# Kernel tuning notes

Measured on AMD Instinct MI355X. Metric: run time of the kernel, lower is better.

The kernel has to match this reference:

```python
import jax, jax.numpy as jnp
import numpy as np

N_USERS = 100000
N_ITEMS = 50000
EMB_DIM = 64
N_LAYERS = 2
N_INTENTS = 128
N_EDGES = 4000000
N_NODES = N_USERS + N_ITEMS


def setup_inputs() -> dict:
    key = jax.random.key(0)
    k1, k2, k3, k4, k5 = jax.random.split(key, 5)
    return {
        "user_emb": 0.1 * jax.random.normal(k1, (N_USERS, EMB_DIM), dtype=jnp.float32),
        "item_emb": 0.1 * jax.random.normal(k2, (N_ITEMS, EMB_DIM), dtype=jnp.float32),
        "intents": jax.random.normal(k3, (EMB_DIM, N_INTENTS), dtype=jnp.float32) * (2.0 / (EMB_DIM + N_INTENTS)) ** 0.5,
        "h_idx": jax.random.randint(k4, (N_EDGES,), 0, N_NODES, dtype=jnp.int64)
        if jax.config.jax_enable_x64 else jax.random.randint(k4, (N_EDGES,), 0, N_NODES, dtype=jnp.int32),
        "t_idx": jax.random.randint(k5, (N_EDGES,), 0, N_NODES, dtype=jnp.int32),
    }


def _spmm(h_idx, t_idx, g_vals, x):
    # y[h] += g_vals * x[t]  (sparse matrix @ dense, COO form)
    gathered = x[t_idx] * g_vals[:, None]  # [E, D]
    return jax.ops.segment_sum(gathered, h_idx, num_segments=N_NODES)


def reference(user_emb, item_emb, intents, h_idx, t_idx):
    # --- _cal_sparse_adj: G = D^{-1/2} A D^{-1/2}, A values are ones ---
    deg = jax.ops.segment_sum(jnp.ones_like(h_idx, dtype=user_emb.dtype), h_idx,
                              num_segments=N_NODES)
    d_inv_sqrt = jnp.where(deg > 0, jax.lax.rsqrt(jnp.maximum(deg, 1e-12)), 0.0)
    g_vals = d_inv_sqrt[h_idx] * d_inv_sqrt[t_idx]  # [E]

    # --- multi-layer propagation with intent-aware embeddings ---
    embs = jnp.concatenate([user_emb, item_emb], axis=0)  # [N, D]
    all_embs = [embs]
    for _ in range(N_LAYERS):
        gnn_embs = _spmm(h_idx, t_idx, g_vals, embs)  # [N, D]
        # intent projection: softmax over intents, reconstruct in emb space
        u, it = embs[:N_USERS], embs[N_USERS:]
        u_int = jax.nn.softmax(u @ intents, axis=1) @ intents.T      # [n_users, D]
        i_int = jax.nn.softmax(it @ intents, axis=1) @ intents.T     # [n_items, D]
        int_embs = jnp.concatenate([u_int, i_int], axis=0)
        embs = gnn_embs + int_embs
        all_embs.append(embs)
    out = jnp.sum(jnp.stack(all_embs, axis=1), axis=1) / len(all_embs)  # mean over layers
    return out
```

## Files before the change

### kernel.cpp

```cpp
#include <hip/hip_runtime.h>
#include <math.h>

#define N_USERS 100000
#define N_ITEMS 50000
#define N_NODES 150000
#define EMB 64
#define NI 128
#define NUM_EDGES 4000000
#define NPAD 150016
#define NB 1172
#define BSTRIDE 4352
#define ETILE 8192
#define EGRID ((NUM_EDGES + ETILE - 1) / ETILE)
#define NT_ALL (NPAD / 16)
#define SBLK (NT_ALL / 4)
#define SENT 150000u

typedef __attribute__((ext_vector_type(8))) short bf16x8;
typedef __attribute__((ext_vector_type(4))) float f32x4;

__device__ __forceinline__ unsigned short f2bf(float f) {
    unsigned int u = __float_as_uint(f);
    u += 0x7FFFu + ((u >> 16) & 1u);
    return (unsigned short)(u >> 16);
}
__device__ __forceinline__ float bflo(unsigned int u) { return __uint_as_float(u << 16); }
__device__ __forceinline__ float bfhi(unsigned int u) { return __uint_as_float(u & 0xFFFF0000u); }


__global__ __launch_bounds__(512) void bucket_scatter(const int* __restrict__ h,
                                                      const int* __restrict__ t,
                                                      int* __restrict__ gcur,
                                                      unsigned int* __restrict__ ebuf) {
    __shared__ int lc[NB];
    __shared__ int lbase[NB];
    __shared__ int lcur[NB];
    int tid = threadIdx.x;
    for (int i = tid; i < NB; i += 512) lc[i] = 0;
    __syncthreads();
    int base = blockIdx.x * ETILE;
#pragma unroll
    for (int k = 0; k < ETILE / 512; ++k) {
        int idx = base + k * 512 + tid;
        if (idx < NUM_EDGES) atomicAdd(&lc[h[idx] >> 7], 1);
    }
    __syncthreads();
    for (int i = tid; i < NB; i += 512) {
        int c = lc[i];
        lbase[i] = c ? (i * BSTRIDE + atomicAdd(&gcur[i], c)) : 0;
        lcur[i] = 0;
    }
    __syncthreads();
#pragma unroll
    for (int k = 0; k < ETILE / 512; ++k) {
        int idx = base + k * 512 + tid;
        if (idx < NUM_EDGES) {
            int hh = h[idx], tt = t[idx];
            int b = hh >> 7;
            int p = lbase[b] + atomicAdd(&lcur[b], 1);
            int lim = b * BSTRIDE + BSTRIDE - 1;
            p = (p <= lim) ? p : lim;
            ebuf[p] = ((unsigned int)(hh & 127) << 18) | (unsigned int)tt;
        }
    }
}


__global__ __launch_bounds__(512) void bucket_csr(const int* __restrict__ gcur,
                                                  unsigned int* __restrict__ ebuf,
                                                  int2* __restrict__ rmeta,
                                                  float* __restrict__ dinv,
                                                  int* __restrict__ perm) {
    __shared__ unsigned int in_s[BSTRIDE];
    __shared__ int cnt_s[128];
    __shared__ int base_s[128];
    __shared__ int sc[128];
    __shared__ int dg[128];
    int b = blockIdx.x, tid = threadIdx.x;
    int s = b * BSTRIDE;
    int n = gcur[b];
    if (n > BSTRIDE) n = BSTRIDE;

    for (int i = tid; i < n; i += 512) in_s[i] = ebuf[s + i];
    if (tid < 128) cnt_s[tid] = 0;
    __syncthreads();
    for (int i = tid; i < n; i += 512) atomicAdd(&cnt_s[in_s[i] >> 18], 1);
    __syncthreads();

    int c = 0, pc = 0;
    if (tid < 128) {
        c = cnt_s[tid];
        pc = (c + 3) & ~3;
        sc[tid] = pc;
        dg[tid] = c;
    }
    __syncthreads();
    for (int off = 1; off < 128; off <<= 1) {
        int tv = 0;
        if (tid < 128 && tid >= off) tv = sc[tid - off];
        __syncthreads();
        if (tid < 128 && tid >= off) sc[tid] += tv;
        __syncthreads();
    }
    if (tid < 128) {
        int excl = sc[tid] - pc;
        base_s[tid] = excl;
        int node = (b << 7) + tid;
        rmeta[node] = make_int2(s + excl, pc);
        dinv[node] = (c > 0) ? rsqrtf((float)c) : 0.0f;
        int tb = tid & ~15;
        int rank = 0;
#pragma unroll
        for (int j = 0; j < 16; ++j) {
            int dj = dg[tb + j];
            rank += (dj > c) || (dj == c && (tb + j) < tid);
        }
        perm[(b << 7) + tb + rank] = node;
        for (int p2 = c; p2 < pc; ++p2) ebuf[s + excl + p2] = SENT;
        cnt_s[tid] = 0;
    }
    __syncthreads();
    for (int i = tid; i < n; i += 512) {
        unsigned int qv = in_s[i];
        int hl = (int)(qv >> 18);
        int p = base_s[hl] + atomicAdd(&cnt_s[hl], 1);
        ebuf[s + p] = qv & 0x3FFFFu;
    }
}


__global__ void init_kernel(const float4* __restrict__ ue4, const float4* __restrict__ ie4,
                            uint2* __restrict__ ebf4, float4* __restrict__ out4) {
    int i = blockIdx.x * blockDim.x + threadIdx.x;
    const int uelems = N_USERS * EMB / 4;
    const int relems = N_NODES * EMB / 4;
    const int total  = NPAD * EMB / 4;
    if (i < total) {
        float4 v = make_float4(0.f, 0.f, 0.f, 0.f);
        if (i < uelems) v = ue4[i];
        else if (i < relems) v = ie4[i - uelems];
        if (i < relems) out4[i] = v;
        unsigned int p0 = ((unsigned int)f2bf(v.y) << 16) | f2bf(v.x);
        unsigned int p1 = ((unsigned int)f2bf(v.w) << 16) | f2bf(v.z);
        ebf4[i] = make_uint2(p0, p1);
    }
}


__global__ __launch_bounds__(256) void wconv(const float* __restrict__ W,
                                             unsigned short* __restrict__ Wt,
                                             unsigned short* __restrict__ W2b) {
    int i = blockIdx.x * 256 + threadIdx.x;
    if (i < EMB * NI) {
        int d = i >> 7, c = i & 127;
        unsigned short b = f2bf(W[i]);
        W2b[i] = b;
        Wt[c * EMB + d] = b;
    }
}


__global__ __launch_bounds__(256, 7) void spmm_intent(const int2* __restrict__ rmeta,
                                                      const unsigned int* __restrict__ col,
                                                      const float* __restrict__ dinv,
                                                      const int* __restrict__ perm,
                                                      const unsigned short* __restrict__ ebf,
                                                      unsigned short* __restrict__ ebfout,
                                                      const unsigned short* __restrict__ Wt,
                                                      const unsigned short* __restrict__ W2b,
                                                      float* __restrict__ acc, float scale) {
    __shared__ __align__(16) float UPool[4][1408];

    int tid = threadIdx.x;
    int wid = tid >> 6, lane = tid & 63;
    int q = lane >> 4, c = lane & 15;
    int qq = lane >> 3, cc = lane & 7;
    int tile = blockIdx.x * 4 + wid;
    if (tile >= NT_ALL) return;
    int rowbase = tile << 4;
    float* fw = &UPool[wid][0];
    unsigned short* pw = (unsigned short*)&UPool[wid][1088];

#pragma unroll 1
    for (int half = 0; half < 2; ++half) {
        int prow = perm[rowbase + half * 8 + qq];
        int2 rm = rmeta[prow];
        int s = rm.x, pcv = rm.y;
        float dr = dinv[prow];

        float a0 = 0.f, a1 = 0.f, a2 = 0.f, a3 = 0.f;
        float a4 = 0.f, a5 = 0.f, a6 = 0.f, a7 = 0.f;
        const unsigned short* eb = ebf + (cc << 3);

        int e0 = (int)(col[s]     & 0x3FFFFu);
        int e1 = (int)(col[s + 1] & 0x3FFFFu);
        int e2 = (int)(col[s + 2] & 0x3FFFFu);
        int e3 = (int)(col[s + 3] & 0x3FFFFu);
        float g0 = dinv[e0], g1 = dinv[e1], g2 = dinv[e2], g3 = dinv[e3];
        uint4 u0 = *(const uint4*)(eb + ((size_t)e0 << 6));
        uint4 u1 = *(const uint4*)(eb + ((size_t)e1 << 6));
        uint4 u2 = *(const uint4*)(eb + ((size_t)e2 << 6));
        uint4 u3 = *(const uint4*)(eb + ((size_t)e3 << 6));
        int f0 = (int)(col[s + 4] & 0x3FFFFu);
        int f1 = (int)(col[s + 5] & 0x3FFFFu);
        int f2 = (int)(col[s + 6] & 0x3FFFFu);
        int f3 = (int)(col[s + 7] & 0x3FFFFu);

        for (int it = 0; it < pcv; it += 4) {
            float h0 = dinv[f0], h1 = dinv[f1], h2 = dinv[f2], h3 = dinv[f3];
            uint4 v0 = *(const uint4*)(eb + ((size_t)f0 << 6));
            uint4 v1 = *(const uint4*)(eb + ((size_t)f1 << 6));
            uint4 v2 = *(const uint4*)(eb + ((size_t)f2 << 6));
            uint4 v3 = *(const uint4*)(eb + ((size_t)f3 << 6));
            int x0 = (int)(col[s + it + 8]  & 0x3FFFFu);
            int x1 = (int)(col[s + it + 9]  & 0x3FFFFu);
            int x2 = (int)(col[s + it + 10] & 0x3FFFFu);
            int x3 = (int)(col[s + it + 11] & 0x3FFFFu);
            a0 = fmaf(g0, bflo(u0.x), a0); a1 = fmaf(g0, bfhi(u0.x), a1);
            a2 = fmaf(g0, bflo(u0.y), a2); a3 = fmaf(g0, bfhi(u0.y), a3);
            a4 = fmaf(g0, bflo(u0.z), a4); a5 = fmaf(g0, bfhi(u0.z), a5);
            a6 = fmaf(g0, bflo(u0.w), a6); a7 = fmaf(g0, bfhi(u0.w), a7);
            a0 = fmaf(g1, bflo(u1.x), a0); a1 = fmaf(g1, bfhi(u1.x), a1);
            a2 = fmaf(g1, bflo(u1.y), a2); a3 = fmaf(g1, bfhi(u1.y), a3);
            a4 = fmaf(g1, bflo(u1.z), a4); a5 = fmaf(g1, bfhi(u1.z), a5);
            a6 = fmaf(g1, bflo(u1.w), a6); a7 = fmaf(g1, bfhi(u1.w), a7);
            a0 = fmaf(g2, bflo(u2.x), a0); a1 = fmaf(g2, bfhi(u2.x), a1);
            a2 = fmaf(g2, bflo(u2.y), a2); a3 = fmaf(g2, bfhi(u2.y), a3);
            a4 = fmaf(g2, bflo(u2.z), a4); a5 = fmaf(g2, bfhi(u2.z), a5);
            a6 = fmaf(g2, bflo(u2.w), a6); a7 = fmaf(g2, bfhi(u2.w), a7);
            a0 = fmaf(g3, bflo(u3.x), a0); a1 = fmaf(g3, bfhi(u3.x), a1);
            a2 = fmaf(g3, bflo(u3.y), a2); a3 = fmaf(g3, bfhi(u3.y), a3);
            a4 = fmaf(g3, bflo(u3.z), a4); a5 = fmaf(g3, bfhi(u3.z), a5);
            a6 = fmaf(g3, bflo(u3.w), a6); a7 = fmaf(g3, bfhi(u3.w), a7);
            u0 = v0; u1 = v1; u2 = v2; u3 = v3;
            g0 = h0; g1 = h1; g2 = h2; g3 = h3;
            f0 = x0; f1 = x1; f2 = x2; f3 = x3;
        }
        int fb = (half * 8 + qq) * 68 + (cc << 3);
        fw[fb + 0] = a0 * dr; fw[fb + 1] = a1 * dr;
        fw[fb + 2] = a2 * dr; fw[fb + 3] = a3 * dr;
        fw[fb + 4] = a4 * dr; fw[fb + 5] = a5 * dr;
        fw[fb + 6] = a6 * dr; fw[fb + 7] = a7 * dr;
    }

    int arow = perm[rowbase + c];
    const unsigned short* erow = ebf + ((size_t)arow << 6);
    bf16x8 A0 = *(const bf16x8*)(erow + (q << 3));
    bf16x8 A1 = *(const bf16x8*)(erow + 32 + (q << 3));
    f32x4 S[8];
#pragma unroll
    for (int t = 0; t < 8; ++t) {
        bf16x8 B0 = *(const bf16x8*)&Wt[(16 * t + c) * EMB + (q << 3)];
        bf16x8 B1 = *(const bf16x8*)&Wt[(16 * t + c) * EMB + 32 + (q << 3)];
        f32x4 z = {0.f, 0.f, 0.f, 0.f};
        z = __builtin_amdgcn_mfma_f32_16x16x32_bf16(A0, B0, z, 0, 0, 0);
        S[t] = __builtin_amdgcn_mfma_f32_16x16x32_bf16(A1, B1, z, 0, 0, 0);
    }

#pragma unroll
    for (int r = 0; r < 4; ++r) {
        float m = S[0][r];
#pragma unroll
        for (int t = 1; t < 8; ++t) m = fmaxf(m, S[t][r]);
        m = fmaxf(m, __shfl_xor(m, 1)); m = fmaxf(m, __shfl_xor(m, 2));
        m = fmaxf(m, __shfl_xor(m, 4)); m = fmaxf(m, __shfl_xor(m, 8));
        float sum = 0.f;
#pragma unroll
        for (int t = 0; t < 8; ++t) { float ex = __expf(S[t][r] - m); S[t][r] = ex; sum += ex; }
        sum += __shfl_xor(sum, 1); sum += __shfl_xor(sum, 2);
        sum += __shfl_xor(sum, 4); sum += __shfl_xor(sum, 8);
        float inv = 1.0f / sum;
#pragma unroll
        for (int t = 0; t < 8; ++t) S[t][r] *= inv;
    }

    f32x4 O0 = {0.f, 0.f, 0.f, 0.f}, O1 = O0, O2 = O0, O3 = O0;
#pragma unroll
    for (int s2 = 0; s2 < 4; ++s2) {
#pragma unroll
        for (int h2 = 0; h2 < 2; ++h2) {
            int t = 2 * s2 + h2;
#pragma unroll
            for (int r = 0; r < 4; ++r) {
                float p = S[t][r];
                unsigned short b = f2bf(p);
                pw[(4 * q + r) * 40 + (h2 << 4) + c] = b;
                S[t][r] = p - bflo((unsigned int)b);
            }
        }
        bf16x8 Pf = *(const bf16x8*)&pw[c * 40 + (q << 3)];
        {
            bf16x8 Bf0 = *(const bf16x8*)&W2b[(c) * NI + (s2 << 5) + (q << 3)];
            bf16x8 Bf1 = *(const bf16x8*)&W2b[(16 + c) * NI + (s2 << 5) + (q << 3)];
            O0 = __builtin_amdgcn_mfma_f32_16x16x32_bf16(Pf, Bf0, O0, 0, 0, 0);
            O1 = __builtin_amdgcn_mfma_f32_16x16x32_bf16(Pf, Bf1, O1, 0, 0, 0);
            bf16x8 Bf2 = *(const bf16x8*)&W2b[(32 + c) * NI + (s2 << 5) + (q << 3)];
            bf16x8 Bf3 = *(const bf16x8*)&W2b[(48 + c) * NI + (s2 << 5) + (q << 3)];
            O2 = __builtin_amdgcn_mfma_f32_16x16x32_bf16(Pf, Bf2, O2, 0, 0, 0);
            O3 = __builtin_amdgcn_mfma_f32_16x16x32_bf16(Pf, Bf3, O3, 0, 0, 0);
        }
#pragma unroll
        for (int h2 = 0; h2 < 2; ++h2) {
            int t = 2 * s2 + h2;
#pragma unroll
            for (int r = 0; r < 4; ++r)
                pw[(4 * q + r) * 40 + (h2 << 4) + c] = f2bf(S[t][r]);
        }
        bf16x8 Pl = *(const bf16x8*)&pw[c * 40 + (q << 3)];
        {
            bf16x8 Bf0 = *(const bf16x8*)&W2b[(c) * NI + (s2 << 5) + (q << 3)];
            bf16x8 Bf1 = *(const bf16x8*)&W2b[(16 + c) * NI + (s2 << 5) + (q << 3)];
            O0 = __builtin_amdgcn_mfma_f32_16x16x32_bf16(Pl, Bf0, O0, 0, 0, 0);
            O1 = __builtin_amdgcn_mfma_f32_16x16x32_bf16(Pl, Bf1, O1, 0, 0, 0);
            bf16x8 Bf2 = *(const bf16x8*)&W2b[(32 + c) * NI + (s2 << 5) + (q << 3)];
            bf16x8 Bf3 = *(const bf16x8*)&W2b[(48 + c) * NI + (s2 << 5) + (q << 3)];
            O2 = __builtin_amdgcn_mfma_f32_16x16x32_bf16(Pl, Bf2, O2, 0, 0, 0);
            O3 = __builtin_amdgcn_mfma_f32_16x16x32_bf16(Pl, Bf3, O3, 0, 0, 0);
        }
    }

    asm volatile("" ::: "memory");

#pragma unroll
    for (int r = 0; r < 4; ++r) {
        int rl = 4 * q + r;
        float* gr = &fw[rl * 68];
        gr[c]      += O0[r];
        gr[16 + c] += O1[r];
        gr[32 + c] += O2[r];
        gr[48 + c] += O3[r];
    }

    {
        int j = lane >> 2, sg = lane & 3;
        int rw = perm[rowbase + j];
        const float* gr = &fw[j * 68 + (sg << 4)];
        float4 x0 = *(const float4*)&gr[0];
        float4 x1 = *(const float4*)&gr[4];
        float4 x2 = *(const float4*)&gr[8];
        float4 x3 = *(const float4*)&gr[12];
        size_t base = ((size_t)rw << 6) + (sg << 4);
        uint4 w0, w1;
        w0.x = (unsigned int)f2bf(x0.x) | ((unsigned int)f2bf(x0.y) << 16);
        w0.y = (unsigned int)f2bf(x0.z) | ((unsigned int)f2bf(x0.w) << 16);
        w0.z = (unsigned int)f2bf(x1.x) | ((unsigned int)f2bf(x1.y) << 16);
        w0.w = (unsigned int)f2bf(x1.z) | ((unsigned int)f2bf(x1.w) << 16);
        w1.x = (unsigned int)f2bf(x2.x) | ((unsigned int)f2bf(x2.y) << 16);
        w1.y = (unsigned int)f2bf(x2.z) | ((unsigned int)f2bf(x2.w) << 16);
        w1.z = (unsigned int)f2bf(x3.x) | ((unsigned int)f2bf(x3.y) << 16);
        w1.w = (unsigned int)f2bf(x3.z) | ((unsigned int)f2bf(x3.w) << 16);
        *(uint4*)(ebfout + base) = w0;
        *(uint4*)(ebfout + base + 8) = w1;
        if (rw < N_NODES) {
            float4* ap = (float4*)(acc + base);
            float4 b0 = ap[0], b1 = ap[1], b2 = ap[2], b3 = ap[3];
            b0.x = (b0.x + x0.x) * scale; b0.y = (b0.y + x0.y) * scale;
            b0.z = (b0.z + x0.z) * scale; b0.w = (b0.w + x0.w) * scale;
            b1.x = (b1.x + x1.x) * scale; b1.y = (b1.y + x1.y) * scale;
            b1.z = (b1.z + x1.z) * scale; b1.w = (b1.w + x1.w) * scale;
            b2.x = (b2.x + x2.x) * scale; b2.y = (b2.y + x2.y) * scale;
            b2.z = (b2.z + x2.z) * scale; b2.w = (b2.w + x2.w) * scale;
            b3.x = (b3.x + x3.x) * scale; b3.y = (b3.y + x3.y) * scale;
            b3.z = (b3.z + x3.z) * scale; b3.w = (b3.w + x3.w) * scale;
            ap[0] = b0; ap[1] = b1; ap[2] = b2; ap[3] = b3;
        }
    }
}


extern "C" void kernel_launch(void* const* d_in, const int* in_sizes, int n_in,
                              void* d_out, int out_size, void* d_ws, size_t ws_size,
                              hipStream_t stream) {
    const float* ue = (const float*)d_in[0];
    const float* ie = (const float*)d_in[1];
    const float* W  = (const float*)d_in[2];
    const int*   h  = (const int*)d_in[3];
    const int*   t  = (const int*)d_in[4];
    float* out = (float*)d_out;

    int*            gcur  = (int*)d_ws;
    int2*           rmeta = (int2*)(gcur + 2048);
    float*          dinv  = (float*)(rmeta + NPAD);
    int*            perm  = (int*)(dinv + NPAD);
    unsigned short* ebfA  = (unsigned short*)(perm + NPAD);
    unsigned short* ebfB  = ebfA + (size_t)NPAD * EMB;
    unsigned int*   ebuf  = (unsigned int*)(ebfB + (size_t)NPAD * EMB);
    unsigned short* Wt    = (unsigned short*)(ebuf + NB * BSTRIDE + 16);
    unsigned short* W2b   = Wt + EMB * NI;

    hipMemsetAsync(gcur, 0, NB * sizeof(int), stream);
    hipMemsetAsync(ebuf + NB * BSTRIDE, 0, 16 * sizeof(unsigned int), stream);
    bucket_scatter<<<EGRID, 512, 0, stream>>>(h, t, gcur, ebuf);
    bucket_csr<<<NB, 512, 0, stream>>>(gcur, ebuf, rmeta, dinv, perm);
    init_kernel<<<(NPAD * EMB / 4 + 255) / 256, 256, 0, stream>>>(
        (const float4*)ue, (const float4*)ie, (uint2*)ebfA, (float4*)out);
    wconv<<<(EMB * NI + 255) / 256, 256, 0, stream>>>(W, Wt, W2b);

    const unsigned int* col = ebuf;
    spmm_intent<<<SBLK, 256, 0, stream>>>(rmeta, col, dinv, perm, ebfA, ebfB, Wt, W2b, out, 1.0f);
    spmm_intent<<<SBLK, 256, 0, stream>>>(rmeta, col, dinv, perm, ebfB, ebfA, Wt, W2b, out, 1.0f / 3.0f);
}
```

Before: 473.2 us.

## Drop degree-sorted row permutation and vectorize column index loads in SpMM

Removes the per-16-row degree-sorting permutation built in bucket_csr, so the SpMM/intent kernel processes rows in natural order with no perm indirection on reads and writes. Column indices are now fetched as one uint4 per group of four instead of four scalar loads, clamped so they stay within the row's padded range. A sched_barrier is added and the occupancy hint drops from 7 to 6 waves. Losing the sort can increase load imbalance among the 8 rows sharing a wave, since rows of different degree now sit together, in exchange for fewer dependent loads and less setup work.

Measured after the change: 458.2 us. -3.2%, faster.

```diff
diff --git a/kernel.cpp b/kernel.cpp
--- a/kernel.cpp
+++ b/kernel.cpp
@@ -69,13 +69,11 @@
 __global__ __launch_bounds__(512) void bucket_csr(const int* __restrict__ gcur,
                                                   unsigned int* __restrict__ ebuf,
                                                   int2* __restrict__ rmeta,
-                                                  float* __restrict__ dinv,
-                                                  int* __restrict__ perm) {
+                                                  float* __restrict__ dinv) {
     __shared__ unsigned int in_s[BSTRIDE];
     __shared__ int cnt_s[128];
     __shared__ int base_s[128];
     __shared__ int sc[128];
-    __shared__ int dg[128];
     int b = blockIdx.x, tid = threadIdx.x;
     int s = b * BSTRIDE;
     int n = gcur[b];
@@ -92,7 +90,6 @@
         c = cnt_s[tid];
         pc = (c + 3) & ~3;
         sc[tid] = pc;
-        dg[tid] = c;
     }
     __syncthreads();
     for (int off = 1; off < 128; off <<= 1) {
@@ -108,14 +105,6 @@
         int node = (b << 7) + tid;
         rmeta[node] = make_int2(s + excl, pc);
         dinv[node] = (c > 0) ? rsqrtf((float)c) : 0.0f;
-        int tb = tid & ~15;
-        int rank = 0;
-#pragma unroll
-        for (int j = 0; j < 16; ++j) {
-            int dj = dg[tb + j];
-            rank += (dj > c) || (dj == c && (tb + j) < tid);
-        }
-        perm[(b << 7) + tb + rank] = node;
         for (int p2 = c; p2 < pc; ++p2) ebuf[s + excl + p2] = SENT;
         cnt_s[tid] = 0;
     }
@@ -160,10 +149,9 @@
 }
 
 
-__global__ __launch_bounds__(256, 7) void spmm_intent(const int2* __restrict__ rmeta,
+__global__ __launch_bounds__(256, 6) void spmm_intent(const int2* __restrict__ rmeta,
                                                       const unsigned int* __restrict__ col,
                                                       const float* __restrict__ dinv,
-                                                      const int* __restrict__ perm,
                                                       const unsigned short* __restrict__ ebf,
                                                       unsigned short* __restrict__ ebfout,
                                                       const unsigned short* __restrict__ Wt,
@@ -183,28 +171,26 @@
 
 #pragma unroll 1
     for (int half = 0; half < 2; ++half) {
-        int prow = perm[rowbase + half * 8 + qq];
-        int2 rm = rmeta[prow];
+        int row = rowbase + half * 8 + qq;
+        int2 rm = rmeta[row];
         int s = rm.x, pcv = rm.y;
-        float dr = dinv[prow];
+        float dr = dinv[row];
 
         float a0 = 0.f, a1 = 0.f, a2 = 0.f, a3 = 0.f;
         float a4 = 0.f, a5 = 0.f, a6 = 0.f, a7 = 0.f;
         const unsigned short* eb = ebf + (cc << 3);
 
-        int e0 = (int)(col[s]     & 0x3FFFFu);
-        int e1 = (int)(col[s + 1] & 0x3FFFFu);
-        int e2 = (int)(col[s + 2] & 0x3FFFFu);
-        int e3 = (int)(col[s + 3] & 0x3FFFFu);
+        uint4 cg0 = *(const uint4*)&col[s];
+        int e0 = (int)(cg0.x & 0x3FFFFu), e1 = (int)(cg0.y & 0x3FFFFu);
+        int e2 = (int)(cg0.z & 0x3FFFFu), e3 = (int)(cg0.w & 0x3FFFFu);
         float g0 = dinv[e0], g1 = dinv[e1], g2 = dinv[e2], g3 = dinv[e3];
         uint4 u0 = *(const uint4*)(eb + ((size_t)e0 << 6));
         uint4 u1 = *(const uint4*)(eb + ((size_t)e1 << 6));
         uint4 u2 = *(const uint4*)(eb + ((size_t)e2 << 6));
         uint4 u3 = *(const uint4*)(eb + ((size_t)e3 << 6));
-        int f0 = (int)(col[s + 4] & 0x3FFFFu);
-        int f1 = (int)(col[s + 5] & 0x3FFFFu);
-        int f2 = (int)(col[s + 6] & 0x3FFFFu);
-        int f3 = (int)(col[s + 7] & 0x3FFFFu);
+        uint4 cg1 = *(const uint4*)&col[s + ((pcv >= 8) ? 4 : 0)];
+        int f0 = (int)(cg1.x & 0x3FFFFu), f1 = (int)(cg1.y & 0x3FFFFu);
+        int f2 = (int)(cg1.z & 0x3FFFFu), f3 = (int)(cg1.w & 0x3FFFFu);
 
         for (int it = 0; it < pcv; it += 4) {
             float h0 = dinv[f0], h1 = dinv[f1], h2 = dinv[f2], h3 = dinv[f3];
@@ -212,10 +198,10 @@
             uint4 v1 = *(const uint4*)(eb + ((size_t)f1 << 6));
             uint4 v2 = *(const uint4*)(eb + ((size_t)f2 << 6));
             uint4 v3 = *(const uint4*)(eb + ((size_t)f3 << 6));
-            int x0 = (int)(col[s + it + 8]  & 0x3FFFFu);
-            int x1 = (int)(col[s + it + 9]  & 0x3FFFFu);
-            int x2 = (int)(col[s + it + 10] & 0x3FFFFu);
-            int x3 = (int)(col[s + it + 11] & 0x3FFFFu);
+            int cb = s + it + 8;
+            int ce = s + pcv - 4;
+            uint4 cgn = *(const uint4*)&col[(cb < ce) ? cb : ce];
+            __builtin_amdgcn_sched_barrier(0);
             a0 = fmaf(g0, bflo(u0.x), a0); a1 = fmaf(g0, bfhi(u0.x), a1);
             a2 = fmaf(g0, bflo(u0.y), a2); a3 = fmaf(g0, bfhi(u0.y), a3);
             a4 = fmaf(g0, bflo(u0.z), a4); a5 = fmaf(g0, bfhi(u0.z), a5);
@@ -234,7 +220,8 @@
             a6 = fmaf(g3, bflo(u3.w), a6); a7 = fmaf(g3, bfhi(u3.w), a7);
             u0 = v0; u1 = v1; u2 = v2; u3 = v3;
             g0 = h0; g1 = h1; g2 = h2; g3 = h3;
-            f0 = x0; f1 = x1; f2 = x2; f3 = x3;
+            f0 = (int)(cgn.x & 0x3FFFFu); f1 = (int)(cgn.y & 0x3FFFFu);
+            f2 = (int)(cgn.z & 0x3FFFFu); f3 = (int)(cgn.w & 0x3FFFFu);
         }
         int fb = (half * 8 + qq) * 68 + (cc << 3);
         fw[fb + 0] = a0 * dr; fw[fb + 1] = a1 * dr;
@@ -243,8 +230,7 @@
         fw[fb + 6] = a6 * dr; fw[fb + 7] = a7 * dr;
     }
 
-    int arow = perm[rowbase + c];
-    const unsigned short* erow = ebf + ((size_t)arow << 6);
+    const unsigned short* erow = ebf + ((size_t)(rowbase + c) << 6);
     bf16x8 A0 = *(const bf16x8*)(erow + (q << 3));
     bf16x8 A1 = *(const bf16x8*)(erow + 32 + (q << 3));
     f32x4 S[8];
@@ -333,7 +319,7 @@
 
     {
         int j = lane >> 2, sg = lane & 3;
-        int rw = perm[rowbase + j];
+        int rw = rowbase + j;
         const float* gr = &fw[j * 68 + (sg << 4)];
         float4 x0 = *(const float4*)&gr[0];
         float4 x1 = *(const float4*)&gr[4];
@@ -381,8 +367,7 @@
     int*            gcur  = (int*)d_ws;
     int2*           rmeta = (int2*)(gcur + 2048);
     float*          dinv  = (float*)(rmeta + NPAD);
-    int*            perm  = (int*)(dinv + NPAD);
-    unsigned short* ebfA  = (unsigned short*)(perm + NPAD);
+    unsigned short* ebfA  = (unsigned short*)(dinv + NPAD);
     unsigned short* ebfB  = ebfA + (size_t)NPAD * EMB;
     unsigned int*   ebuf  = (unsigned int*)(ebfB + (size_t)NPAD * EMB);
     unsigned short* Wt    = (unsigned short*)(ebuf + NB * BSTRIDE + 16);
@@ -391,12 +376,12 @@
     hipMemsetAsync(gcur, 0, NB * sizeof(int), stream);
     hipMemsetAsync(ebuf + NB * BSTRIDE, 0, 16 * sizeof(unsigned int), stream);
     bucket_scatter<<<EGRID, 512, 0, stream>>>(h, t, gcur, ebuf);
-    bucket_csr<<<NB, 512, 0, stream>>>(gcur, ebuf, rmeta, dinv, perm);
+    bucket_csr<<<NB, 512, 0, stream>>>(gcur, ebuf, rmeta, dinv);
     init_kernel<<<(NPAD * EMB / 4 + 255) / 256, 256, 0, stream>>>(
         (const float4*)ue, (const float4*)ie, (uint2*)ebfA, (float4*)out);
     wconv<<<(EMB * NI + 255) / 256, 256, 0, stream>>>(W, Wt, W2b);
 
     const unsigned int* col = ebuf;
-    spmm_intent<<<SBLK, 256, 0, stream>>>(rmeta, col, dinv, perm, ebfA, ebfB, Wt, W2b, out, 1.0f);
-    spmm_intent<<<SBLK, 256, 0, stream>>>(rmeta, col, dinv, perm, ebfB, ebfA, Wt, W2b, out, 1.0f / 3.0f);
-}
+    spmm_intent<<<SBLK, 256, 0, stream>>>(rmeta, col, dinv, ebfA, ebfB, Wt, W2b, out, 1.0f);
+    spmm_intent<<<SBLK, 256, 0, stream>>>(rmeta, col, dinv, ebfB, ebfA, Wt, W2b, out, 1.0f / 3.0f);
+}
```
